# Performance work log

Measured on AMD Instinct MI355X. Metric: run time of the kernel, lower is better.

Reference implementation:

```python
import math
import jax, jax.numpy as jnp
import numpy as np

IMG_W = 640
IMG_H = 360
STRIDE = 32
NUM_OFFSETS = 72
FH = IMG_H // STRIDE   # 11
FW = IMG_W // STRIDE   # 20
AFC = 64               # anchor_feat_channels
BB_C = 512             # backbone channels
B = 8

LEFT_ANGLES = [72., 60., 49., 39., 30., 22.]
RIGHT_ANGLES = [108., 120., 131., 141., 150., 158.]
BOTTOM_ANGLES = [165., 150., 141., 131., 120., 108., 100., 90., 80., 72., 60., 49., 39., 30., 15.]


def _make_anchors():
    ys = np.linspace(1.0, 0.0, NUM_OFFSETS)
    cys = np.linspace(1.0, 0.0, FH)

    def side(angles, nb, x=None, y=None):
        if x is None:
            starts = [(xx, y) for xx in np.linspace(1.0, 0.0, nb)]
        else:
            starts = [(x, yy) for yy in np.linspace(1.0, 0.0, nb)]
        A = np.zeros((nb * len(angles), 2 + NUM_OFFSETS))
        C = np.zeros((nb * len(angles), 2 + FH))
        k = 0
        for sx, sy in starts:
            for ang in angles:
                t = math.tan(ang * math.pi / 180.0)
                A[k, 0] = 1 - sy; A[k, 1] = sx
                A[k, 2:] = (sx + (sy - ys) / t) * IMG_W
                C[k, 0] = 1 - sy; C[k, 1] = sx
                C[k, 2:] = (sx + (sy - cys) / t) * IMG_W
                k += 1
        return A, C

    la, lc = side(LEFT_ANGLES, 72, x=0.0)
    ba, bc = side(BOTTOM_ANGLES, 128, y=1.0)
    ra, rc = side(RIGHT_ANGLES, 72, x=1.0)
    anchors = np.concatenate([la, ba, ra]).astype(np.float32)   # [P, 74]
    cuts = np.concatenate([lc, bc, rc])                          # [P, 2+FH]
    unclamped = np.flip(np.round(cuts[:, 2:] / STRIDE).astype(np.int64), axis=1)
    cut_x = np.clip(unclamped, 0, FW - 1).astype(np.int32)       # [P, FH]
    invalid = (unclamped < 0) | (unclamped > FW)                 # [P, FH]
    return anchors, cut_x, invalid


def setup_inputs() -> dict:
    key = jax.random.key(0)
    ks = jax.random.split(key, 6)
    anchors, cut_x, invalid = _make_anchors()
    P = anchors.shape[0]          # 2784
    D = AFC * FH                  # 704
    std = 1e-3
    return {
        'x': jax.random.normal(ks[0], (B, BB_C, FH, FW), jnp.float32),
        'conv_w': jax.random.normal(ks[1], (AFC, BB_C), jnp.float32) * std,
        'conv_b': jnp.zeros((AFC,), jnp.float32),
        'att_w': jax.random.normal(ks[2], (P - 1, D), jnp.float32) * std,
        'att_b': jnp.zeros((P - 1,), jnp.float32),
        'cls_w': jax.random.normal(ks[3], (2, 2 * D), jnp.float32) * std,
        'cls_b': jnp.zeros((2,), jnp.float32),
        'reg_w': jax.random.normal(ks[4], (NUM_OFFSETS + 1, 2 * D), jnp.float32) * std,
        'reg_b': jnp.zeros((NUM_OFFSETS + 1,), jnp.float32),
        'anchors': jnp.asarray(anchors),
        'cut_x': jnp.asarray(cut_x),
        'invalid': jnp.asarray(invalid),
    }


def reference(x, conv_w, conv_b, att_w, att_b, cls_w, cls_b, reg_w, reg_b,
              anchors, cut_x, invalid):
    Bb = x.shape[0]
    P = anchors.shape[0]
    D = AFC * FH
    # 1x1 conv: [B, BB_C, FH, FW] -> [B, AFC, FH, FW]
    f = jnp.einsum('bchw,oc->bohw', x, conv_w) + conv_b[None, :, None, None]
    # cut_anchor_features: per-anchor column gather, zero out-of-image rows
    rows = jnp.arange(FH)[None, :]                 # [1, FH]
    g = f[:, :, rows, cut_x]                       # [B, AFC, P, FH]
    g = jnp.where(invalid[None, None, :, :], 0.0, g)
    feat = jnp.transpose(g, (0, 2, 1, 3)).reshape(Bb, P, D)   # [B, P, D]
    # attention over proposals
    scores = feat @ att_w.T + att_b                # [B, P, P-1]
    att = jax.nn.softmax(scores, axis=-1)
    # scatter attention into off-diagonal of [B, P, P] (diag = 0)
    k = jnp.arange(P - 1)
    i = jnp.arange(P)
    cols = k[None, :] + (k[None, :] >= i[:, None]).astype(k.dtype)   # [P, P-1]
    att_mat = jnp.zeros((Bb, P, P), feat.dtype).at[:, i[:, None], cols].set(att)
    # attention_features[b,p,:] = sum_j att_mat[b,p,j] * feat[b,j,:]
    att_feat = jnp.einsum('bpj,bjd->bpd', att_mat, feat)
    cat = jnp.concatenate([att_feat, feat], axis=-1)   # [B, P, 2D]
    cls_logits = cat @ cls_w.T + cls_b                  # [B, P, 2]
    reg = cat @ reg_w.T + reg_b                         # [B, P, 73]
    reg_prop = jnp.broadcast_to(anchors[None], (Bb, P, anchors.shape[1]))
    reg_prop = reg_prop.at[:, :, 1:].add(reg)
    return reg_prop[..., 2:], reg_prop[..., 0], reg_prop[..., 1], cls_logits
```

## Files before the change

### kernel.cpp

```cpp
#include <hip/hip_runtime.h>
#include <stdint.h>

typedef short short8 __attribute__((ext_vector_type(8)));
typedef float floatx4 __attribute__((ext_vector_type(4)));
typedef unsigned short ushort_t;
typedef unsigned char u8;

constexpr int cFH = 11, cFW = 20, cP = 2784, cPM1 = 2783, cD = 704;
constexpr int cAFC = 64, cBBC = 512, cNB = 8, cNPAD = 2816, cM = 22272;
constexpr int cFTR = 768;

static __device__ __forceinline__ float bf2f(unsigned short u) {
  union { unsigned u32; float f; } v; v.u32 = ((unsigned)u) << 16; return v.f;
}
static __device__ __forceinline__ unsigned short f2bf(float f) {
  union { float f; unsigned u; } v; v.f = f;
  unsigned r = v.u + 0x7fffu + ((v.u >> 16) & 1u);
  return (unsigned short)(r >> 16);
}
static __device__ __forceinline__ u8 f2fp8(float f) {
  int v = __builtin_amdgcn_cvt_pk_fp8_f32(f, 0.f, 0, false);
  return (u8)(v & 0xff);
}
static __device__ __forceinline__ int imin(int a, int b) { return a < b ? a : b; }
static __device__ __forceinline__ int swz8(int row) { return ((row >> 1) & 3) << 3; }

static __device__ __forceinline__ int xcd_swz(int orig, int total) {
  int q = total >> 3, r = total & 7;
  int xcd = orig & 7, pos = orig >> 3;
  return (xcd < r ? xcd * (q + 1) : r * (q + 1) + (xcd - r) * q) + pos;
}

static __device__ __forceinline__ void gload16(const void* g, void* l) {
  __builtin_amdgcn_global_load_lds(
      (const __attribute__((address_space(1))) unsigned int*)g,
      (__attribute__((address_space(3))) unsigned int*)l, 16, 0, 0);
}

static __device__ __forceinline__ floatx4 mfma_fp8(long a, long b, floatx4 c) {
  return __builtin_amdgcn_mfma_f32_16x16x32_fp8_fp8(a, b, c, 0, 0, 0);
}

#define PIPE_BAR4() asm volatile("s_waitcnt vmcnt(4)\n\ts_barrier" ::: "memory")
#define PIPE_BAR2() asm volatile("s_waitcnt vmcnt(2)\n\ts_barrier" ::: "memory")
#define PIPE_BAR0() asm volatile("s_waitcnt vmcnt(0)\n\ts_barrier" ::: "memory")

constexpr float kFeatScale = 16.f;
constexpr float kAttwScale = 64.f;
constexpr float kSInv = 1.f / (kFeatScale * kAttwScale);

__global__ void k_conv4(const float* __restrict__ x, const float* __restrict__ w,
                        const float* __restrict__ bias, float* __restrict__ f) {
  int idx = blockIdx.x * 256 + threadIdx.x;
  if (idx >= cNB * 16 * 220) return;
  int yx = idx % 220;
  int og = (idx / 220) % 16;
  int b  = idx / (220 * 16);
  int o0 = og * 4;
  const float* xp = x + (size_t)b * cBBC * 220 + yx;
  const float* w0 = w + (size_t)o0 * cBBC;
  const float* w1 = w0 + cBBC;
  const float* w2 = w1 + cBBC;
  const float* w3 = w2 + cBBC;
  float a0 = 0.f, a1 = 0.f, a2 = 0.f, a3 = 0.f;
#pragma unroll 4
  for (int c = 0; c < cBBC; ++c) {
    float xv = xp[(size_t)c * 220];
    a0 += xv * w0[c]; a1 += xv * w1[c]; a2 += xv * w2[c]; a3 += xv * w3[c];
  }
  f[((size_t)(b * cAFC + o0) * 220) + yx]     = a0 + bias[o0];
  f[((size_t)(b * cAFC + o0 + 1) * 220) + yx] = a1 + bias[o0 + 1];
  f[((size_t)(b * cAFC + o0 + 2) * 220) + yx] = a2 + bias[o0 + 2];
  f[((size_t)(b * cAFC + o0 + 3) * 220) + yx] = a3 + bias[o0 + 3];
}

__global__ void k_gatherT(const float* __restrict__ f, const int* __restrict__ cut_x,
                          const unsigned char* __restrict__ invalid,
                          ushort_t* __restrict__ feat, u8* __restrict__ feat8,
                          u8* __restrict__ featT8, int b_base) {
  __shared__ ushort_t tile[64][66];
  int bz = blockIdx.z;
  int b  = b_base + bz;
  int p0 = blockIdx.x * 64, d0 = blockIdx.y * 64;
  int t = threadIdx.x;
#pragma unroll
  for (int m = 0; m < 16; ++m) {
    int idx = t + m * 256; int r = idx >> 6, c = idx & 63;
    int p = p0 + r, d = d0 + c;
    ushort_t v = 0;
    if (p < cP) {
      int o = d / cFH, i2 = d - o * cFH;
      int cx = cut_x[p * cFH + i2];
      float vv = invalid[p * cFH + i2] ? 0.f
               : f[((size_t)(b * cAFC + o) * cFH + i2) * cFW + cx];
      v = f2bf(vv);
      feat[((size_t)b * cP + p) * cD + d] = v;
      feat8[((size_t)b * cP + p) * cD + d] = f2fp8(vv * kFeatScale);
    }
    tile[r][c] = v;
  }
  __syncthreads();
#pragma unroll
  for (int m = 0; m < 16; ++m) {
    int idx = t + m * 256; int r = idx >> 6, c = idx & 63;
    float tv = bf2f(tile[c][r]);
    featT8[((size_t)bz * cFTR + d0 + r) * cNPAD + p0 + c] = f2fp8(tv * kFeatScale);
  }
}

__global__ void k_prep_w(const float* __restrict__ att_w, const float* __restrict__ reg_w,
                         const float* __restrict__ cls_w,
                         u8* __restrict__ attw8, ushort_t* __restrict__ Wt) {
  int idx = blockIdx.x * 256 + threadIdx.x;
  constexpr int n1 = cNPAD * cD;
  if (idx < n1) {
    int r = idx / cD;
    attw8[idx] = (r < cPM1) ? f2fp8(att_w[idx] * kAttwScale) : (u8)0;
  } else {
    int j = idx - n1;
    if (j < 80 * 1408) {
      int r = j / 1408, k = j % 1408;
      float v = 0.f;
      if (r < 73) v = reg_w[(size_t)r * 1408 + k];
      else if (r < 75) v = cls_w[(size_t)(r - 73) * 1408 + k];
      Wt[j] = f2bf(v);
    }
  }
}

__global__ void k_denom(const float* __restrict__ partial, float* __restrict__ denom, int n) {
  int i = blockIdx.x * 256 + threadIdx.x;
  if (i >= n) return;
  float s = 0.f;
#pragma unroll 4
  for (int q = 0; q < 44; ++q) s += partial[(size_t)q * cM + i];
  denom[i] = s;
}

__global__ __launch_bounds__(256, 4) void k_gemm_s2(
    const u8* __restrict__ feat8, const u8* __restrict__ attw8,
    const float* __restrict__ att_b, u8* __restrict__ Pp8,
    float* __restrict__ partial, int m_base, int m_count, int pp_base) {
  __shared__ __align__(16) u8 lds[3][8192];
  int wg = xcd_swz(blockIdx.x, gridDim.x);
  int ntile = wg % 22, mtile = wg / 22;
  int tid = threadIdx.x;
  int w = tid >> 6, l = tid & 63, lr = l & 15, lg = l >> 4;
  int wr = (w >> 1) * 64, wc = (w & 1) * 64;
  int m0 = m_base + mtile * 128;
  int n0 = ntile * 128;
  int rmaxA = m_base + m_count - 1;

  int srow = w * 32 + (l >> 1);
  int shalf = (l & 1) * 16;
  const u8* a0 = feat8 + (size_t)imin(m0 + srow, rmaxA) * cD + shalf;
  const u8* b0 = attw8 + (size_t)(n0 + srow) * cD + shalf;
  int w1024 = w * 1024;

  int offA[4], offB[4];
#pragma unroll
  for (int mt = 0; mt < 4; ++mt) offA[mt] = (wr + mt * 16 + lr) * 32 + lg * 8;
#pragma unroll
  for (int nt = 0; nt < 4; ++nt) offB[nt] = 4096 + (wc + nt * 16 + lr) * 32 + lg * 8;

  floatx4 acc[4][4];
  floatx4 zero = {0.f, 0.f, 0.f, 0.f};
#pragma unroll
  for (int a = 0; a < 4; ++a)
#pragma unroll
    for (int q = 0; q < 4; ++q) acc[a][q] = zero;

  auto stage = [&](int buf) {
    u8* L = &lds[buf][0];
    gload16(a0, L + w1024);
    gload16(b0, L + 4096 + w1024);
    a0 += 32; b0 += 32;
  };

  stage(0); stage(1);
  int c0 = 0, c1 = 1, c2 = 2;
  constexpr int NK = cD / 32;
  for (int t = 0; t < NK; ++t) {
    if (t + 1 < NK) PIPE_BAR2(); else PIPE_BAR0();
    if (t + 2 < NK) stage(c2);
    const u8* Lc = lds[c0];
    long av[4], bv[4];
#pragma unroll
    for (int mt = 0; mt < 4; ++mt) av[mt] = *(const long*)(Lc + offA[mt]);
#pragma unroll
    for (int nt = 0; nt < 4; ++nt) bv[nt] = *(const long*)(Lc + offB[nt]);
#pragma unroll
    for (int mt = 0; mt < 4; ++mt)
#pragma unroll
      for (int nt = 0; nt < 4; ++nt)
        acc[mt][nt] = mfma_fp8(av[mt], bv[nt], acc[mt][nt]);
    int tmp = c0; c0 = c1; c1 = c2; c2 = tmp;
  }

  int w1 = w & 1;
  float ab[4]; int kc[4];
#pragma unroll
  for (int nt = 0; nt < 4; ++nt) {
    int k = n0 + wc + nt * 16 + lr;
    kc[nt] = k;
    ab[nt] = (k < cPM1) ? att_b[k] : -1e30f;
  }
#pragma unroll
  for (int mt = 0; mt < 4; ++mt) {
#pragma unroll
    for (int r = 0; r < 4; ++r) {
      int i = m0 + wr + mt * 16 + lg * 4 + r;
      int il = i - pp_base;
      bool rowok = (unsigned)(i - m_base) < (unsigned)m_count;
      int pl = i % cP;
      size_t rowbase = (size_t)il * cNPAD;
      float s = 0.f;
#pragma unroll
      for (int nt = 0; nt < 4; ++nt) {
        int k = kc[nt];
        float e = __expf(acc[mt][nt][r] * kSInv + ab[nt]);
        s += e;
        int j = k + (k >= pl ? 1 : 0);
        if (rowok && j < cNPAD) Pp8[rowbase + j] = f2fp8(e);
        if (rowok && (k == pl || (k == cPM1 - 1 && pl == cPM1)))
          Pp8[rowbase + pl] = 0;
      }
      s += __shfl_xor(s, 1); s += __shfl_xor(s, 2);
      s += __shfl_xor(s, 4); s += __shfl_xor(s, 8);
      if (lr == 0 && rowok)
        partial[(size_t)(ntile * 2 + w1) * cM + il] = s;
    }
  }
}

__global__ __launch_bounds__(256, 4) void k_gemm_pv2(
    const u8* __restrict__ Pp8, const u8* __restrict__ featT8,
    const float* __restrict__ denom, ushort_t* __restrict__ af,
    int b_base, int pp_base, int ft_base, int af_base) {
  __shared__ __align__(16) u8 lds[3][8192];
  int wg = xcd_swz(blockIdx.x, gridDim.x);
  int ntile = wg % 6;
  int t6 = wg / 6;
  int mtile = t6 % 22;
  int b = b_base + t6 / 22;
  int tid = threadIdx.x;
  int w = tid >> 6, l = tid & 63, lr = l & 15, lg = l >> 4;
  int wr = (w >> 1) * 64, wc = (w & 1) * 64;
  int m0l = mtile * 128;
  int n0 = ntile * 128;
  int bP = b * cP - pp_base;

  int srow = w * 32 + (l >> 1);
  int shalf = (l & 1) * 16;
  const u8* a0 = Pp8 + (size_t)(bP + imin(m0l + srow, cP - 1)) * cNPAD + shalf;
  const u8* b0 = featT8 + ((size_t)(b - ft_base) * cFTR + n0 + srow) * cNPAD + shalf;
  int w1024 = w * 1024;

  int offA[4], offB[4];
#pragma unroll
  for (int mt = 0; mt < 4; ++mt) offA[mt] = (wr + mt * 16 + lr) * 32 + lg * 8;
#pragma unroll
  for (int nt = 0; nt < 4; ++nt) offB[nt] = 4096 + (wc + nt * 16 + lr) * 32 + lg * 8;

  floatx4 acc[4][4];
  floatx4 zero = {0.f, 0.f, 0.f, 0.f};
#pragma unroll
  for (int a = 0; a < 4; ++a)
#pragma unroll
    for (int q = 0; q < 4; ++q) acc[a][q] = zero;

  auto stage = [&](int buf) {
    u8* L = &lds[buf][0];
    gload16(a0, L + w1024);
    gload16(b0, L + 4096 + w1024);
    a0 += 32; b0 += 32;
  };

  stage(0); stage(1);
  int c0 = 0, c1 = 1, c2 = 2;
  constexpr int NK = cP / 32;
  for (int t = 0; t < NK; ++t) {
    if (t + 1 < NK) PIPE_BAR2(); else PIPE_BAR0();
    if (t + 2 < NK) stage(c2);
    const u8* Lc = lds[c0];
    long av[4], bv[4];
#pragma unroll
    for (int mt = 0; mt < 4; ++mt) av[mt] = *(const long*)(Lc + offA[mt]);
#pragma unroll
    for (int nt = 0; nt < 4; ++nt) bv[nt] = *(const long*)(Lc + offB[nt]);
#pragma unroll
    for (int mt = 0; mt < 4; ++mt)
#pragma unroll
      for (int nt = 0; nt < 4; ++nt)
        acc[mt][nt] = mfma_fp8(av[mt], bv[nt], acc[mt][nt]);
    int tmp = c0; c0 = c1; c1 = c2; c2 = tmp;
  }

#pragma unroll
  for (int mt = 0; mt < 4; ++mt)
#pragma unroll
    for (int r = 0; r < 4; ++r) {
      int p = m0l + wr + mt * 16 + lg * 4 + r;
      if (p >= cP) continue;
      float dn = denom[bP + p] * kFeatScale;
#pragma unroll
      for (int nt = 0; nt < 4; ++nt) {
        int dd = n0 + wc + nt * 16 + lr;
        if (dd < cD)
          af[((size_t)(b * cP + p) - af_base) * cD + dd] = f2bf(acc[mt][nt][r] / dn);
      }
    }
}

__global__ __launch_bounds__(256, 4) void k_gemm_out(
    const ushort_t* __restrict__ af, const ushort_t* __restrict__ feat,
    const ushort_t* __restrict__ Wt,
    const float* __restrict__ reg_b, const float* __restrict__ cls_b,
    const float* __restrict__ anchors,
    float* __restrict__ out0, float* __restrict__ out1,
    float* __restrict__ out2, float* __restrict__ out3,
    int m_base, int m_count, int af_base) {
  __shared__ __align__(16) ushort_t sA[3][4096];
  int tid = threadIdx.x;
  int w = tid >> 6, l = tid & 63, lr = l & 15, lg = l >> 4;
  int wr = w * 32;
  int m0 = m_base + blockIdx.x * 128;
  int lastRow = m_base + m_count - 1;

  int srow = w * 16 + (l >> 2);
  int scol = ((l & 3) * 8) ^ swz8(srow);
  const ushort_t* pa0_af = af + (size_t)(imin(m0 + srow, lastRow) - af_base) * cD + scol;
  const ushort_t* pa1_af = af + (size_t)(imin(m0 + 64 + srow, lastRow) - af_base) * cD + scol;
  const ushort_t* pa0_f  = feat + (size_t)imin(m0 + srow, lastRow) * cD + scol;
  const ushort_t* pa1_f  = feat + (size_t)imin(m0 + 64 + srow, lastRow) * cD + scol;
  int lbase = w * 512;

  int offO[2];
#pragma unroll
  for (int mt = 0; mt < 2; ++mt) {
    int row = wr + mt * 16 + lr;
    offO[mt] = row * 32 + ((lg * 8) ^ swz8(row));
  }

  floatx4 zero = {0.f, 0.f, 0.f, 0.f};
  floatx4 acc[2][5];
#pragma unroll
  for (int a = 0; a < 2; ++a)
#pragma unroll
    for (int q = 0; q < 5; ++q) acc[a][q] = zero;

  auto stageA = [&](int buf, int kk) {
    const ushort_t *s0, *s1;
    if (kk < 22) { s0 = pa0_af + kk * 32; s1 = pa1_af + kk * 32; }
    else         { s0 = pa0_f + (kk - 22) * 32; s1 = pa1_f + (kk - 22) * 32; }
    gload16(s0, &sA[buf][lbase]);
    gload16(s1, &sA[buf][lbase + 2048]);
  };

  stageA(0, 0); stageA(1, 1);
  int c0 = 0, c1 = 1, c2 = 2;
  for (int kk = 0; kk < 44; ++kk) {
    if (kk + 1 < 44) PIPE_BAR2(); else PIPE_BAR0();
    int kb = kk * 32 + lg * 8;
    short8 bvv[5];
#pragma unroll
    for (int nt = 0; nt < 5; ++nt)
      bvv[nt] = *(const short8*)(Wt + (size_t)(nt * 16 + lr) * 1408 + kb);
    if (kk + 2 < 44) stageA(c2, kk + 2);
    short8 avv[2];
#pragma unroll
    for (int mt = 0; mt < 2; ++mt)
      avv[mt] = *(const short8*)&sA[c0][offO[mt]];
#pragma unroll
    for (int nt = 0; nt < 5; ++nt)
#pragma unroll
      for (int mt = 0; mt < 2; ++mt)
        acc[mt][nt] = __builtin_amdgcn_mfma_f32_16x16x32_bf16(avv[mt], bvv[nt], acc[mt][nt], 0, 0, 0);
    int tmp = c0; c0 = c1; c1 = c2; c2 = tmp;
  }

#pragma unroll
  for (int mt = 0; mt < 2; ++mt)
#pragma unroll
    for (int nt = 0; nt < 5; ++nt)
#pragma unroll
      for (int r = 0; r < 4; ++r) {
        int i = m0 + wr + mt * 16 + lg * 4 + r;
        if (i - m_base >= m_count) continue;
        int o = nt * 16 + lr;
        int p = i % cP;
        float v = acc[mt][nt][r];
        const float* an = anchors + (size_t)p * 74;
        if (o == 0)        { out2[i] = an[1] + v + reg_b[0]; out1[i] = an[0]; }
        else if (o < 73)   { out0[(size_t)i * 72 + (o - 1)] = an[1 + o] + v + reg_b[o]; }
        else if (o == 73)  { out3[(size_t)i * 2]     = v + cls_b[0]; }
        else if (o == 74)  { out3[(size_t)i * 2 + 1] = v + cls_b[1]; }
      }
}

extern "C" void kernel_launch(void* const* d_in, const int* in_sizes, int n_in,
                              void* d_out, int out_size, void* d_ws, size_t ws_size,
                              hipStream_t stream) {
  const float* x       = (const float*)d_in[0];
  const float* conv_w  = (const float*)d_in[1];
  const float* conv_b  = (const float*)d_in[2];
  const float* att_w   = (const float*)d_in[3];
  const float* att_b   = (const float*)d_in[4];
  const float* cls_w   = (const float*)d_in[5];
  const float* cls_b   = (const float*)d_in[6];
  const float* reg_w   = (const float*)d_in[7];
  const float* reg_b   = (const float*)d_in[8];
  const float* anchors = (const float*)d_in[9];
  const int*   cut_x   = (const int*)d_in[10];
  const unsigned char* invalid = (const unsigned char*)d_in[11];
  float* out0 = (float*)d_out;
  float* out1 = out0 + (size_t)cM * 72;
  float* out2 = out1 + cM;
  float* out3 = out2 + cM;

  size_t off = 0;
  char* base = (char*)d_ws;
  auto carve = [&](size_t bytes) -> void* {
    void* r = base + off; off += (bytes + 255) & ~(size_t)255; return r;
  };
  float* fbuf    = (float*)carve((size_t)cNB * cAFC * cFH * cFW * 4);
  ushort_t* feat = (ushort_t*)carve((size_t)cM * cD * 2);
  u8* feat8      = (u8*)carve((size_t)cM * cD);
  u8* attw8      = (u8*)carve((size_t)cNPAD * cD);
  ushort_t* Wt   = (ushort_t*)carve((size_t)80 * 1408 * 2);
  float* partial = (float*)carve((size_t)44 * cM * 4);
  float* denom   = (float*)carve((size_t)cM * 4);

  size_t featT_full = (size_t)cNB * cFTR * cNPAD, featT_one = (size_t)cFTR * cNPAD;
  size_t af_full    = (size_t)cM * cD * 2,        af_one    = (size_t)cP * cD * 2;
  size_t pp_full    = (size_t)cM * cNPAD,         pp_one    = (size_t)cNPAD * cNPAD;

  size_t needA = off + featT_full + af_full + pp_full;
  size_t needB = off + featT_full + af_full + pp_one;
  int mode = (ws_size >= needA) ? 0 : ((ws_size >= needB) ? 1 : 2);

  u8 *featT8, *Pp8; ushort_t *af;
  if (mode == 0)      { featT8 = (u8*)carve(featT_full); af = (ushort_t*)carve(af_full); Pp8 = (u8*)carve(pp_full); }
  else if (mode == 1) { featT8 = (u8*)carve(featT_full); af = (ushort_t*)carve(af_full); Pp8 = (u8*)carve(pp_one); }
  else                { featT8 = (u8*)carve(featT_one);  af = (ushort_t*)carve(af_one);  Pp8 = (u8*)carve(pp_one); }

  k_conv4<<<(cNB * 16 * 220 + 255) / 256, 256, 0, stream>>>(x, conv_w, conv_b, fbuf);
  k_prep_w<<<(cNPAD * cD + 80 * 1408 + 255) / 256, 256, 0, stream>>>(att_w, reg_w, cls_w, attw8, Wt);

  if (mode == 0) {
    k_gatherT<<<dim3(44, 11, 8), 256, 0, stream>>>(fbuf, cut_x, invalid, feat, feat8, featT8, 0);
    k_gemm_s2<<<174 * 22, 256, 0, stream>>>(feat8, attw8, att_b, Pp8, partial, 0, cM, 0);
    k_denom<<<(cM + 255) / 256, 256, 0, stream>>>(partial, denom, cM);
    k_gemm_pv2<<<8 * 22 * 6, 256, 0, stream>>>(Pp8, featT8, denom, af, 0, 0, 0, 0);
    k_gemm_out<<<174, 256, 0, stream>>>(af, feat, Wt, reg_b, cls_b, anchors,
                                        out0, out1, out2, out3, 0, cM, 0);
  } else if (mode == 1) {
    k_gatherT<<<dim3(44, 11, 8), 256, 0, stream>>>(fbuf, cut_x, invalid, feat, feat8, featT8, 0);
    for (int b = 0; b < cNB; ++b) {
      k_gemm_s2<<<22 * 22, 256, 0, stream>>>(feat8, attw8, att_b, Pp8, partial, b * cP, cP, b * cP);
      k_denom<<<(cP + 255) / 256, 256, 0, stream>>>(partial, denom, cP);
      k_gemm_pv2<<<22 * 6, 256, 0, stream>>>(Pp8, featT8, denom, af, b, b * cP, 0, 0);
    }
    k_gemm_out<<<174, 256, 0, stream>>>(af, feat, Wt, reg_b, cls_b, anchors,
                                        out0, out1, out2, out3, 0, cM, 0);
  } else {
    for (int b = 0; b < cNB; ++b) {
      k_gatherT<<<dim3(44, 11, 1), 256, 0, stream>>>(fbuf, cut_x, invalid, feat, feat8, featT8, b);
      k_gemm_s2<<<22 * 22, 256, 0, stream>>>(feat8, attw8, att_b, Pp8, partial, b * cP, cP, b * cP);
      k_denom<<<(cP + 255) / 256, 256, 0, stream>>>(partial, denom, cP);
      k_gemm_pv2<<<22 * 6, 256, 0, stream>>>(Pp8, featT8, denom, af, b, b * cP, b, b * cP);
      k_gemm_out<<<22, 256, 0, stream>>>(af, feat, Wt, reg_b, cls_b, anchors,
                                         out0, out1, out2, out3, b * cP, cP, b * cP);
    }
  }
}
```

Before: 384.4 us.

## Store fp8 GEMM operands in 16-row tiled layout for contiguous 512-byte loads

The fp8 operand buffers (feat8, attw8, featT8, Pp8) move from row-major storage to a tiled layout where each 16-row by 32-column block is contiguous. Each workgroup's global-to-LDS staging then reads contiguous 512-byte chunks instead of strided 16-byte pieces from many rows. This should improve coalescing and DRAM/L2 efficiency in both attention GEMMs. The cost is scattered byte writes in the producer kernels (gather, weight prep, softmax-exp epilogue), and the LDS fragment offsets have to match the new layout.

```diff
diff --git a/kernel.cpp b/kernel.cpp
--- a/kernel.cpp
+++ b/kernel.cpp
@@ -9,6 +9,9 @@
 constexpr int cFH = 11, cFW = 20, cP = 2784, cPM1 = 2783, cD = 704;
 constexpr int cAFC = 64, cBBC = 512, cNB = 8, cNPAD = 2816, cM = 22272;
 constexpr int cFTR = 768;
+constexpr int cK16_704  = 704 * 16;
+constexpr int cK16_2816 = 2816 * 16;
+constexpr size_t cFTbatch = (size_t)(cFTR / 16) * cK16_2816;
 
 static __device__ __forceinline__ float bf2f(unsigned short u) {
   union { unsigned u32; float f; } v; v.u32 = ((unsigned)u) << 16; return v.f;
@@ -25,6 +28,11 @@
 static __device__ __forceinline__ int imin(int a, int b) { return a < b ? a : b; }
 static __device__ __forceinline__ int swz8(int row) { return ((row >> 1) & 3) << 3; }
 
+static __device__ __forceinline__ size_t tiled_addr(int R, int c, int k16) {
+  return (size_t)(R >> 4) * k16 + (size_t)(((c >> 5) << 9) + (((c >> 3) & 3) << 7) +
+         ((R & 15) << 3) + (c & 7));
+}
+
 static __device__ __forceinline__ int xcd_swz(int orig, int total) {
   int q = total >> 3, r = total & 7;
   int xcd = orig & 7, pos = orig >> 3;
@@ -41,7 +49,6 @@
   return __builtin_amdgcn_mfma_f32_16x16x32_fp8_fp8(a, b, c, 0, 0, 0);
 }
 
-#define PIPE_BAR4() asm volatile("s_waitcnt vmcnt(4)\n\ts_barrier" ::: "memory")
 #define PIPE_BAR2() asm volatile("s_waitcnt vmcnt(2)\n\ts_barrier" ::: "memory")
 #define PIPE_BAR0() asm volatile("s_waitcnt vmcnt(0)\n\ts_barrier" ::: "memory")
 
@@ -95,7 +102,7 @@
                : f[((size_t)(b * cAFC + o) * cFH + i2) * cFW + cx];
       v = f2bf(vv);
       feat[((size_t)b * cP + p) * cD + d] = v;
-      feat8[((size_t)b * cP + p) * cD + d] = f2fp8(vv * kFeatScale);
+      feat8[tiled_addr(b * cP + p, d, cK16_704)] = f2fp8(vv * kFeatScale);
     }
     tile[r][c] = v;
   }
@@ -104,7 +111,8 @@
   for (int m = 0; m < 16; ++m) {
     int idx = t + m * 256; int r = idx >> 6, c = idx & 63;
     float tv = bf2f(tile[c][r]);
-    featT8[((size_t)bz * cFTR + d0 + r) * cNPAD + p0 + c] = f2fp8(tv * kFeatScale);
+    featT8[(size_t)bz * cFTbatch + tiled_addr(d0 + r, p0 + c, cK16_2816)] =
+        f2fp8(tv * kFeatScale);
   }
 }
 
@@ -114,8 +122,8 @@
   int idx = blockIdx.x * 256 + threadIdx.x;
   constexpr int n1 = cNPAD * cD;
   if (idx < n1) {
-    int r = idx / cD;
-    attw8[idx] = (r < cPM1) ? f2fp8(att_w[idx] * kAttwScale) : (u8)0;
+    int r = idx / cD, k = idx % cD;
+    attw8[tiled_addr(r, k, cK16_704)] = (r < cPM1) ? f2fp8(att_w[idx] * kAttwScale) : (u8)0;
   } else {
     int j = idx - n1;
     if (j < 80 * 1408) {
@@ -149,32 +157,32 @@
   int wr = (w >> 1) * 64, wc = (w & 1) * 64;
   int m0 = m_base + mtile * 128;
   int n0 = ntile * 128;
-  int rmaxA = m_base + m_count - 1;
-
-  int srow = w * 32 + (l >> 1);
-  int shalf = (l & 1) * 16;
-  const u8* a0 = feat8 + (size_t)imin(m0 + srow, rmaxA) * cD + shalf;
-  const u8* b0 = attw8 + (size_t)(n0 + srow) * cD + shalf;
+
+  int q = w * 64 + l;
+  int rbq = q >> 5, sq = (q & 31) * 16;
+  int rbA = imin((m0 >> 4) + rbq, (cM >> 4) - 1);
+  const u8* a0 = feat8 + (size_t)rbA * cK16_704 + sq;
+  const u8* b0 = attw8 + (size_t)((n0 >> 4) + rbq) * cK16_704 + sq;
   int w1024 = w * 1024;
 
   int offA[4], offB[4];
 #pragma unroll
-  for (int mt = 0; mt < 4; ++mt) offA[mt] = (wr + mt * 16 + lr) * 32 + lg * 8;
-#pragma unroll
-  for (int nt = 0; nt < 4; ++nt) offB[nt] = 4096 + (wc + nt * 16 + lr) * 32 + lg * 8;
+  for (int mt = 0; mt < 4; ++mt) offA[mt] = ((wr >> 4) + mt) * 512 + lg * 128 + lr * 8;
+#pragma unroll
+  for (int nt = 0; nt < 4; ++nt) offB[nt] = 4096 + ((wc >> 4) + nt) * 512 + lg * 128 + lr * 8;
 
   floatx4 acc[4][4];
   floatx4 zero = {0.f, 0.f, 0.f, 0.f};
 #pragma unroll
   for (int a = 0; a < 4; ++a)
 #pragma unroll
-    for (int q = 0; q < 4; ++q) acc[a][q] = zero;
+    for (int qq = 0; qq < 4; ++qq) acc[a][qq] = zero;
 
   auto stage = [&](int buf) {
     u8* L = &lds[buf][0];
     gload16(a0, L + w1024);
     gload16(b0, L + 4096 + w1024);
-    a0 += 32; b0 += 32;
+    a0 += 512; b0 += 512;
   };
 
   stage(0); stage(1);
@@ -213,7 +221,6 @@
       int il = i - pp_base;
       bool rowok = (unsigned)(i - m_base) < (unsigned)m_count;
       int pl = i % cP;
-      size_t rowbase = (size_t)il * cNPAD;
       float s = 0.f;
 #pragma unroll
       for (int nt = 0; nt < 4; ++nt) {
@@ -221,9 +228,9 @@
         float e = __expf(acc[mt][nt][r] * kSInv + ab[nt]);
         s += e;
         int j = k + (k >= pl ? 1 : 0);
-        if (rowok && j < cNPAD) Pp8[rowbase + j] = f2fp8(e);
+        if (rowok && j < cNPAD) Pp8[tiled_addr(il, j, cK16_2816)] = f2fp8(e);
         if (rowok && (k == pl || (k == cPM1 - 1 && pl == cPM1)))
-          Pp8[rowbase + pl] = 0;
+          Pp8[tiled_addr(il, pl, cK16_2816)] = 0;
       }
       s += __shfl_xor(s, 1); s += __shfl_xor(s, 2);
       s += __shfl_xor(s, 4); s += __shfl_xor(s, 8);
@@ -236,7 +243,7 @@
 __global__ __launch_bounds__(256, 4) void k_gemm_pv2(
     const u8* __restrict__ Pp8, const u8* __restrict__ featT8,
     const float* __restrict__ denom, ushort_t* __restrict__ af,
-    int b_base, int pp_base, int ft_base, int af_base) {
+    int b_base, int pp_base, int ft_base, int af_base, int rbMaxPp) {
   __shared__ __align__(16) u8 lds[3][8192];
   int wg = xcd_swz(blockIdx.x, gridDim.x);
   int ntile = wg % 6;
@@ -250,30 +257,32 @@
   int n0 = ntile * 128;
   int bP = b * cP - pp_base;
 
-  int srow = w * 32 + (l >> 1);
-  int shalf = (l & 1) * 16;
-  const u8* a0 = Pp8 + (size_t)(bP + imin(m0l + srow, cP - 1)) * cNPAD + shalf;
-  const u8* b0 = featT8 + ((size_t)(b - ft_base) * cFTR + n0 + srow) * cNPAD + shalf;
+  int q = w * 64 + l;
+  int rbq = q >> 5, sq = (q & 31) * 16;
+  int rbA = imin(((bP + m0l) >> 4) + rbq, rbMaxPp);
+  const u8* a0 = Pp8 + (size_t)rbA * cK16_2816 + sq;
+  const u8* b0 = featT8 + (size_t)(b - ft_base) * cFTbatch
+               + (size_t)((n0 >> 4) + rbq) * cK16_2816 + sq;
   int w1024 = w * 1024;
 
   int offA[4], offB[4];
 #pragma unroll
-  for (int mt = 0; mt < 4; ++mt) offA[mt] = (wr + mt * 16 + lr) * 32 + lg * 8;
-#pragma unroll
-  for (int nt = 0; nt < 4; ++nt) offB[nt] = 4096 + (wc + nt * 16 + lr) * 32 + lg * 8;
+  for (int mt = 0; mt < 4; ++mt) offA[mt] = ((wr >> 4) + mt) * 512 + lg * 128 + lr * 8;
+#pragma unroll
+  for (int nt = 0; nt < 4; ++nt) offB[nt] = 4096 + ((wc >> 4) + nt) * 512 + lg * 128 + lr * 8;
 
   floatx4 acc[4][4];
   floatx4 zero = {0.f, 0.f, 0.f, 0.f};
 #pragma unroll
   for (int a = 0; a < 4; ++a)
 #pragma unroll
-    for (int q = 0; q < 4; ++q) acc[a][q] = zero;
+    for (int qq = 0; qq < 4; ++qq) acc[a][qq] = zero;
 
   auto stage = [&](int buf) {
     u8* L = &lds[buf][0];
     gload16(a0, L + w1024);
     gload16(b0, L + 4096 + w1024);
-    a0 += 32; b0 += 32;
+    a0 += 512; b0 += 512;
   };
 
   stage(0); stage(1);
@@ -444,6 +453,8 @@
   else if (mode == 1) { featT8 = (u8*)carve(featT_full); af = (ushort_t*)carve(af_full); Pp8 = (u8*)carve(pp_one); }
   else                { featT8 = (u8*)carve(featT_one);  af = (ushort_t*)carve(af_one);  Pp8 = (u8*)carve(pp_one); }
 
+  int rbMaxPp = (mode == 0) ? (cM >> 4) - 1 : (cNPAD >> 4) - 1;
+
   k_conv4<<<(cNB * 16 * 220 + 255) / 256, 256, 0, stream>>>(x, conv_w, conv_b, fbuf);
   k_prep_w<<<(cNPAD * cD + 80 * 1408 + 255) / 256, 256, 0, stream>>>(att_w, reg_w, cls_w, attw8, Wt);
 
@@ -451,7 +462,7 @@
     k_gatherT<<<dim3(44, 11, 8), 256, 0, stream>>>(fbuf, cut_x, invalid, feat, feat8, featT8, 0);
     k_gemm_s2<<<174 * 22, 256, 0, stream>>>(feat8, attw8, att_b, Pp8, partial, 0, cM, 0);
     k_denom<<<(cM + 255) / 256, 256, 0, stream>>>(partial, denom, cM);
-    k_gemm_pv2<<<8 * 22 * 6, 256, 0, stream>>>(Pp8, featT8, denom, af, 0, 0, 0, 0);
+    k_gemm_pv2<<<8 * 22 * 6, 256, 0, stream>>>(Pp8, featT8, denom, af, 0, 0, 0, 0, rbMaxPp);
     k_gemm_out<<<174, 256, 0, stream>>>(af, feat, Wt, reg_b, cls_b, anchors,
                                         out0, out1, out2, out3, 0, cM, 0);
   } else if (mode == 1) {
@@ -459,7 +470,7 @@
     for (int b = 0; b < cNB; ++b) {
       k_gemm_s2<<<22 * 22, 256, 0, stream>>>(feat8, attw8, att_b, Pp8, partial, b * cP, cP, b * cP);
       k_denom<<<(cP + 255) / 256, 256, 0, stream>>>(partial, denom, cP);
-      k_gemm_pv2<<<22 * 6, 256, 0, stream>>>(Pp8, featT8, denom, af, b, b * cP, 0, 0);
+      k_gemm_pv2<<<22 * 6, 256, 0, stream>>>(Pp8, featT8, denom, af, b, b * cP, 0, 0, rbMaxPp);
     }
     k_gemm_out<<<174, 256, 0, stream>>>(af, feat, Wt, reg_b, cls_b, anchors,
                                         out0, out1, out2, out3, 0, cM, 0);
@@ -468,7 +479,7 @@
       k_gatherT<<<dim3(44, 11, 1), 256, 0, stream>>>(fbuf, cut_x, invalid, feat, feat8, featT8, b);
       k_gemm_s2<<<22 * 22, 256, 0, stream>>>(feat8, attw8, att_b, Pp8, partial, b * cP, cP, b * cP);
       k_denom<<<(cP + 255) / 256, 256, 0, stream>>>(partial, denom, cP);
-      k_gemm_pv2<<<22 * 6, 256, 0, stream>>>(Pp8, featT8, denom, af, b, b * cP, b, b * cP);
+      k_gemm_pv2<<<22 * 6, 256, 0, stream>>>(Pp8, featT8, denom, af, b, b * cP, b, b * cP, rbMaxPp);
       k_gemm_out<<<22, 256, 0, stream>>>(af, feat, Wt, reg_b, cls_b, anchors,
                                          out0, out1, out2, out3, b * cP, cP, b * cP);
     }
```

After: 321.4 us, median of 2. 16.4% less time.
